# Kernel tuning notes

Hardware: AMD Instinct MI355X
Metric: run time of the kernel (lower is better)

The kernel has to match this reference:

```python
import jax, jax.numpy as jnp
import numpy as np

EPS = 1e-6
K = 20  # n_knn from init


def _vnt_weight(W):
    # VNT linear: rows normalized to sum to 1 (which_norm_VNT='norm') for translation equivariance
    return W / jnp.sum(W, axis=1, keepdims=True)


def _lin(W, x):
    # apply [out,in] weight over channel axis 1 of x: [B, C_in, 3, ...] -> [B, C_out, 3, ...]
    return jnp.einsum('oi,bi...->bo...', W, x)


def _vn_lrelu(x, Wf, Wd, vnt=False):
    # VN(T)LinearLeakyReLU with negative_slope=0.0, no batchnorm. Vector axis is axis 2.
    Wp = _vnt_weight(Wf) if vnt else Wf
    p = _lin(Wp, x)
    d = _lin(Wd, x)
    dot = jnp.sum(p * d, axis=2, keepdims=True)
    dsq = jnp.sum(d * d, axis=2, keepdims=True)
    return jnp.where(dot >= 0, p, p - (dot / (dsq + EPS)) * d)


def _knn(pts, k):
    # pts: [B,N,3] -> indices of k nearest (self included), via -||xi-xj||^2 top_k
    sq = jnp.sum(pts * pts, axis=-1)                      # [B,N]
    inner = jnp.einsum('bnd,bmd->bnm', pts, pts)          # [B,N,N]
    neg_dist = 2.0 * inner - sq[:, :, None] - sq[:, None, :]
    return jax.lax.top_k(neg_dist, k)[1]                  # [B,N,k]


def _graph_feature_cross(x, k):
    # x: [B,3,N] -> edge features [B, 3(feat: nbr-ctr, ctr, cross), 3(vec), N, k]
    pts = jnp.transpose(x, (0, 2, 1))                     # [B,N,3]
    idx = _knn(pts, k)                                    # [B,N,k]
    nbr = jax.vmap(lambda p, i: p[i])(pts, idx)           # [B,N,k,3]
    ctr = jnp.broadcast_to(pts[:, :, None, :], nbr.shape)
    cross = jnp.cross(nbr, ctr)
    feat = jnp.stack([nbr - ctr, ctr, cross], axis=3)     # [B,N,k,3feat,3vec]
    return jnp.transpose(feat, (0, 3, 4, 1, 2))           # [B,3feat,3vec,N,k]


def _forward(x, Wpos_f, Wpos_d, Wc1_f, Wc1_d, Wc2_f, Wc2_d, Wt_f, Wt_d, W1_f, W1_d, W2_f, W2_d, W3):
    feat = _graph_feature_cross(x, K)                     # [B,3,3,N,K]
    h = _vn_lrelu(feat, Wpos_f, Wpos_d, vnt=True)         # [B,64,3,N,K]
    h = h.mean(axis=-1)                                   # mean pool over k -> [B,64,3,N]
    x2 = _vn_lrelu(h, Wc1_f, Wc1_d, vnt=True)             # conv_center_
    xc = _vn_lrelu(x2, Wc2_f, Wc2_d, vnt=True)            # conv_center
    tx = _vn_lrelu(xc, Wt_f, Wt_d, vnt=True)              # conv_trans [B,12,3,N]
    trans_latent = tx.mean(axis=-1)                       # [B,12,3]
    h = h - xc                                            # center features
    h = _vn_lrelu(h, W1_f, W1_d)                          # conv1
    h = _vn_lrelu(h, W2_f, W2_d)                          # conv2
    h = _lin(W3, h)                                       # conv3 (plain VNLinear) [B,116,3,N]
    rot_latent = h.mean(axis=-1)                          # [B,116,3]
    return jnp.concatenate([rot_latent, trans_latent], axis=1)  # [B,128,3]


def setup_inputs() -> dict:
    key = jax.random.key(0)
    ks = jax.random.split(key, 16)
    B, N, C = 4, 4096, 64
    ROT = 116  # c_dim - trans_c_dim

    def w(k, o, i):
        return jax.random.normal(k, (o, i), jnp.float32) * 0.1

    def wt(k, o, i):
        # VNT weights: row sums kept near 1 so normalization is well-conditioned
        return jax.random.normal(k, (o, i), jnp.float32) * 0.02 + 1.0 / i

    return {
        'x': jax.random.normal(ks[0], (B, 3, N), jnp.float32),
        'Wpos_f': wt(ks[1], C, 3), 'Wpos_d': w(ks[2], C, 3),
        'Wc1_f': wt(ks[3], C, C), 'Wc1_d': w(ks[4], C, C),
        'Wc2_f': wt(ks[5], C, C), 'Wc2_d': w(ks[6], C, C),
        'Wt_f': wt(ks[7], 12, C), 'Wt_d': w(ks[8], 12, C),
        'W1_f': w(ks[9], C, C), 'W1_d': w(ks[10], C, C),
        'W2_f': w(ks[11], C, C), 'W2_d': w(ks[12], C, C),
        'W3': w(ks[13], ROT, C),
    }


def reference(x, Wpos_f, Wpos_d, Wc1_f, Wc1_d, Wc2_f, Wc2_d, Wt_f, Wt_d, W1_f, W1_d, W2_f, W2_d, W3):
    return _forward(x, Wpos_f, Wpos_d, Wc1_f, Wc1_d, Wc2_f, Wc2_d, Wt_f, Wt_d, W1_f, W1_d, W2_f, W2_d, W3)
```

## Files before the change

### kernel.cpp

```cpp
#include <hip/hip_runtime.h>

#define NPTS 4096
#define BATCH 4
#define KNN 20
#define ROT 116

__device__ __forceinline__ void vn_lrelu3(float p[3], const float d[3]) {
  float dot = p[0]*d[0] + p[1]*d[1] + p[2]*d[2];
  if (dot < 0.0f) {
    float dsq = d[0]*d[0] + d[1]*d[1] + d[2]*d[2];
    float r = dot / (dsq + 1e-6f);
    p[0] -= r*d[0]; p[1] -= r*d[1]; p[2] -= r*d[2];
  }
}

__global__ __launch_bounds__(256) void knn_kernel(const float* __restrict__ x,
                                                  int* __restrict__ knn) {
  const int row = blockIdx.x;
  const int b = row >> 12, i = row & (NPTS - 1);
  const float* __restrict__ xb = x + b * 3 * NPTS;
  const float cx = xb[i], cy = xb[NPTS + i], cz = xb[2 * NPTS + i];
  const int t = threadIdx.x;
  const int j0 = t << 4;

  __shared__ unsigned int hist[2048];
  __shared__ unsigned int ld_[384];
  __shared__ int lj_[384];
  __shared__ unsigned int lcount;
  __shared__ int s_B;
  __shared__ int wtot[4];

  for (int k = t; k < 2048; k += 256) hist[k] = 0u;
  if (t == 0) lcount = 0u;
  __syncthreads();

  unsigned int db[16];
#pragma unroll
  for (int q = 0; q < 4; ++q) {
    const float4 px = *(const float4*)(xb + j0 + 4 * q);
    const float4 py = *(const float4*)(xb + NPTS + j0 + 4 * q);
    const float4 pz = *(const float4*)(xb + 2 * NPTS + j0 + 4 * q);
    float dx, dy, dz, dd;
    dx = px.x - cx; dy = py.x - cy; dz = pz.x - cz;
    dd = dx*dx + dy*dy + dz*dz; db[4*q+0] = __float_as_uint(dd);
    dx = px.y - cx; dy = py.y - cy; dz = pz.y - cz;
    dd = dx*dx + dy*dy + dz*dz; db[4*q+1] = __float_as_uint(dd);
    dx = px.z - cx; dy = py.z - cy; dz = pz.z - cz;
    dd = dx*dx + dy*dy + dz*dz; db[4*q+2] = __float_as_uint(dd);
    dx = px.w - cx; dy = py.w - cy; dz = pz.w - cz;
    dd = dx*dx + dy*dy + dz*dz; db[4*q+3] = __float_as_uint(dd);
  }
#pragma unroll
  for (int s = 0; s < 16; ++s) atomicAdd(&hist[db[s] >> 20], 1u);
  __syncthreads();

  int v = 0;
#pragma unroll
  for (int s = 0; s < 8; ++s) v += (int)hist[t * 8 + s];
  const int myps = v;
  const int lane = t & 63;
#pragma unroll
  for (int off = 1; off < 64; off <<= 1) {
    int n = __shfl_up(v, off);
    if (lane >= off) v += n;
  }
  if (lane == 63) wtot[t >> 6] = v;
  __syncthreads();
  int woff = 0;
#pragma unroll
  for (int w = 0; w < 4; ++w) if (w < (t >> 6)) woff += wtot[w];
  const int cum_in = v + woff;
  const int cum_ex = cum_in - myps;
  if (cum_ex < KNN && cum_in >= KNN) {
    int cum = cum_ex, B = t * 8;
    for (int s = 0; s < 8; ++s) {
      const int hh = (int)hist[t * 8 + s];
      if (cum + hh >= KNN) { B = t * 8 + s; break; }
      cum += hh;
    }
    s_B = B;
  }
  __syncthreads();
  const unsigned int Bb = (unsigned int)s_B;
#pragma unroll
  for (int s = 0; s < 16; ++s) {
    if ((db[s] >> 20) <= Bb) {
      unsigned int pos = atomicAdd(&lcount, 1u);
      if (pos < 384u) { ld_[pos] = db[s]; lj_[pos] = j0 + s; }
    }
  }
  __syncthreads();
  const int n = min((int)lcount, 384);
  for (int idx = t; idx < n; idx += 256) {
    const unsigned int kd = ld_[idx]; const int kj = lj_[idx];
    int rank = 0;
    for (int m = 0; m < n; ++m) {
      const unsigned int md = ld_[m];
      rank += (md < kd || (md == kd && lj_[m] < kj)) ? 1 : 0;
    }
    if (rank < KNN) knn[row * KNN + rank] = kj;
  }
}

__global__ __launch_bounds__(256) void edge_kernel(const float* __restrict__ x,
                                                   const int* __restrict__ knn,
                                                   const float* __restrict__ Wf,
                                                   const float* __restrict__ Wd,
                                                   float* __restrict__ h) {
  const int g = threadIdx.x >> 6;
  const int lane = threadIdx.x & 63;
  const int p = (blockIdx.x << 2) + g;
  const int b = p >> 12, i = p & (NPTS - 1);
  const float* xb = x + b * 3 * NPTS;
  const float cx = xb[i], cy = xb[NPTS + i], cz = xb[2 * NPTS + i];
  __shared__ float e[4][KNN][3][3];
  if (lane < KNN) {
    int j = knn[p * KNN + lane];
    float nx = xb[j], ny = xb[NPTS + j], nz = xb[2 * NPTS + j];
    e[g][lane][0][0] = nx - cx; e[g][lane][0][1] = ny - cy; e[g][lane][0][2] = nz - cz;
    e[g][lane][1][0] = cx;      e[g][lane][1][1] = cy;      e[g][lane][1][2] = cz;
    e[g][lane][2][0] = ny * cz - nz * cy;
    e[g][lane][2][1] = nz * cx - nx * cz;
    e[g][lane][2][2] = nx * cy - ny * cx;
  }
  __syncthreads();
  const int c = lane;
  float f0 = Wf[c * 3 + 0], f1 = Wf[c * 3 + 1], f2 = Wf[c * 3 + 2];
  float s = 1.0f / (f0 + f1 + f2);
  f0 *= s; f1 *= s; f2 *= s;
  const float d0 = Wd[c * 3 + 0], d1 = Wd[c * 3 + 1], d2 = Wd[c * 3 + 2];
  float a0 = 0.f, a1 = 0.f, a2 = 0.f;
  for (int k = 0; k < KNN; ++k) {
    float pv[3], dv[3];
#pragma unroll
    for (int v = 0; v < 3; ++v) {
      pv[v] = f0 * e[g][k][0][v] + f1 * e[g][k][1][v] + f2 * e[g][k][2][v];
      dv[v] = d0 * e[g][k][0][v] + d1 * e[g][k][1][v] + d2 * e[g][k][2][v];
    }
    vn_lrelu3(pv, dv);
    a0 += pv[0]; a1 += pv[1]; a2 += pv[2];
  }
  const float inv = 1.0f / KNN;
  float* hp = h + p * 192 + c * 3;
  hp[0] = a0 * inv; hp[1] = a1 * inv; hp[2] = a2 * inv;
}

template<bool VNT, int MODE>
__global__ __launch_bounds__(256) void layer_batch(
    const float* in, float* out, float* aux,
    const float* __restrict__ Wf, const float* __restrict__ Wd) {
  __shared__ float wfT[64][65], wdT[64][65];
  __shared__ float act[4][4][64][4];
  const int t = threadIdx.x, q = t >> 6, c = t & 63;
  for (int e = t; e < 4096; e += 256) {
    wfT[e & 63][e >> 6] = Wf[e];
    wdT[e & 63][e >> 6] = Wd[e];
  }
  __syncthreads();
  if (VNT) {
    if (t < 64) {
      float s = 0.f;
      for (int i = 0; i < 64; ++i) s += wfT[i][t];
      s = 1.0f / s;
      for (int i = 0; i < 64; ++i) wfT[i][t] *= s;
    }
    __syncthreads();
  }
  const int pbase = (blockIdx.x * 4 + q) * 8;
  float r0 = 0.f, r1 = 0.f, r2 = 0.f;
  for (int pass = 0; pass < 2; ++pass) {
    const int p0 = pbase + pass * 4;
#pragma unroll
    for (int p = 0; p < 4; ++p) {
      const float* ip = in + (size_t)(p0 + p) * 192 + c * 3;
      *(float4*)act[q][p][c] = make_float4(ip[0], ip[1], ip[2], 0.f);
    }
    __builtin_amdgcn_wave_barrier();
    float af[12], ad[12];
#pragma unroll
    for (int e = 0; e < 12; ++e) { af[e] = 0.f; ad[e] = 0.f; }
    for (int i = 0; i < 64; ++i) {
      const float wfv = wfT[i][c];
      const float wdv = wdT[i][c];
#pragma unroll
      for (int p = 0; p < 4; ++p) {
        const float4 hv = *(const float4*)act[q][p][i];
        af[p*3+0] += wfv * hv.x; af[p*3+1] += wfv * hv.y; af[p*3+2] += wfv * hv.z;
        ad[p*3+0] += wdv * hv.x; ad[p*3+1] += wdv * hv.y; ad[p*3+2] += wdv * hv.z;
      }
    }
    __builtin_amdgcn_wave_barrier();
#pragma unroll
    for (int p = 0; p < 4; ++p) {
      float pf[3] = { af[p*3+0], af[p*3+1], af[p*3+2] };
      float pd[3] = { ad[p*3+0], ad[p*3+1], ad[p*3+2] };
      vn_lrelu3(pf, pd);
      const size_t ofs = (size_t)(p0 + p) * 192 + c * 3;
      if (MODE == 0) {
        out[ofs+0] = pf[0]; out[ofs+1] = pf[1]; out[ofs+2] = pf[2];
      } else if (MODE == 1) {
        const float h0 = aux[ofs+0], h1 = aux[ofs+1], h2 = aux[ofs+2];
        aux[ofs+0] = h0 - pf[0]; aux[ofs+1] = h1 - pf[1]; aux[ofs+2] = h2 - pf[2];
        out[ofs+0] = pf[0]; out[ofs+1] = pf[1]; out[ofs+2] = pf[2];
      } else {
        r0 += pf[0]; r1 += pf[1]; r2 += pf[2];
      }
    }
    __builtin_amdgcn_wave_barrier();
  }
  if (MODE == 2) {
    *(float4*)act[q][0][c] = make_float4(r0, r1, r2, 0.f);
    __syncthreads();
    if (t < 192) {
      const int cc = t / 3, vv = t - cc * 3;
      out[blockIdx.x * 192 + t] =
          act[0][0][cc][vv] + act[1][0][cc][vv] + act[2][0][cc][vv] + act[3][0][cc][vv];
    }
  }
}

__global__ __launch_bounds__(256) void trans_kernel(
    const float* __restrict__ xc,
    const float* __restrict__ Wtf, const float* __restrict__ Wtd,
    float* __restrict__ trans_part) {
  __shared__ float wtf[12][65], wtd[12][65];
  __shared__ float xpt[4][64][4];
  __shared__ float tred[4][12][3];
  const int t = threadIdx.x, q = t >> 6, l = t & 63;
  for (int e = t; e < 768; e += 256) {
    wtf[e >> 6][e & 63] = Wtf[e]; wtd[e >> 6][e & 63] = Wtd[e];
  }
  __syncthreads();
  if (t < 12) {
    float s = 0.f;
    for (int i = 0; i < 64; ++i) s += wtf[t][i];
    s = 1.0f / s;
    for (int i = 0; i < 64; ++i) wtf[t][i] *= s;
  }
  __syncthreads();
  const int cch = l >> 2, v = l & 3;
  const bool act = (cch < 12) && (v < 3);
  float ta = 0.f;
  const int pbase = (blockIdx.x * 4 + q) * 8;
  for (int g = 0; g < 8; ++g) {
    const float* xp = xc + (size_t)(pbase + g) * 192 + l * 3;
    xpt[q][l][0] = xp[0]; xpt[q][l][1] = xp[1]; xpt[q][l][2] = xp[2];
    __builtin_amdgcn_wave_barrier();
    float pf = 0.f, pd = 0.f;
    if (act) {
      for (int i = 0; i < 64; ++i) {
        const float a = xpt[q][i][v];
        pf += wtf[cch][i] * a;
        pd += wtd[cch][i] * a;
      }
    }
    float pp = pf * pd, dd = pd * pd;
    pp += __shfl_xor(pp, 1); pp += __shfl_xor(pp, 2);
    dd += __shfl_xor(dd, 1); dd += __shfl_xor(dd, 2);
    if (pp < 0.f) pf -= (pp / (dd + 1e-6f)) * pd;
    ta += pf;
    __builtin_amdgcn_wave_barrier();
  }
  if (act) { tred[q][cch][v] = ta; }
  __syncthreads();
  if (t < 36) {
    const int cc = t / 3, vv = t - cc * 3;
    trans_part[blockIdx.x * 36 + t] =
        tred[0][cc][vv] + tred[1][cc][vv] + tred[2][cc][vv] + tred[3][cc][vv];
  }
}

__global__ __launch_bounds__(384) void finalize_kernel(const float* __restrict__ rot_part,
                                                       const float* __restrict__ trans_part,
                                                       const float* __restrict__ W3,
                                                       float* __restrict__ out) {
  const int b = blockIdx.x;
  const int t = threadIdx.x;
  __shared__ float hsum[64][3];
  if (t < 192) {
    float s = 0.f;
    for (int blk = 0; blk < 128; ++blk)
      s += rot_part[(b * 128 + blk) * 192 + t];
    hsum[t / 3][t % 3] = s * (1.0f / NPTS);
  } else if (t < 228) {
    const int tt = t - 192;
    float s = 0.f;
    for (int blk = 0; blk < 128; ++blk)
      s += trans_part[(b * 128 + blk) * 36 + tt];
    out[b * 384 + 348 + tt] = s * (1.0f / NPTS);
  }
  __syncthreads();
  if (t < 348) {
    const int ch = t / 3, v = t - ch * 3;
    float s = 0.f;
    for (int i = 0; i < 64; ++i) s += W3[ch * 64 + i] * hsum[i][v];
    out[b * 384 + t] = s;
  }
}

extern "C" void kernel_launch(void* const* d_in, const int* in_sizes, int n_in,
                              void* d_out, int out_size, void* d_ws, size_t ws_size,
                              hipStream_t stream) {
  (void)in_sizes; (void)n_in; (void)out_size; (void)ws_size;
  const float* x     = (const float*)d_in[0];
  const float* Wposf = (const float*)d_in[1];
  const float* Wposd = (const float*)d_in[2];
  const float* Wc1f  = (const float*)d_in[3];
  const float* Wc1d  = (const float*)d_in[4];
  const float* Wc2f  = (const float*)d_in[5];
  const float* Wc2d  = (const float*)d_in[6];
  const float* Wtf   = (const float*)d_in[7];
  const float* Wtd   = (const float*)d_in[8];
  const float* W1f   = (const float*)d_in[9];
  const float* W1d   = (const float*)d_in[10];
  const float* W2f   = (const float*)d_in[11];
  const float* W2d   = (const float*)d_in[12];
  const float* W3    = (const float*)d_in[13];
  float* out = (float*)d_out;

  char* ws = (char*)d_ws;
  int*   knn        = (int*)ws;
  float* P          = (float*)(ws + 1310720);
  float* Q          = (float*)(ws + 13893632);
  float* trans_part = (float*)(ws + 26476544);
  float* rot_part   = (float*)(ws + 26550272);

  knn_kernel<<<BATCH * NPTS, 256, 0, stream>>>(x, knn);
  edge_kernel<<<BATCH * NPTS / 4, 256, 0, stream>>>(x, knn, Wposf, Wposd, P);
  layer_batch<true, 0><<<512, 256, 0, stream>>>(P, Q, nullptr, Wc1f, Wc1d);
  layer_batch<true, 1><<<512, 256, 0, stream>>>(Q, Q, P, Wc2f, Wc2d);
  trans_kernel<<<512, 256, 0, stream>>>(Q, Wtf, Wtd, trans_part);
  layer_batch<false, 0><<<512, 256, 0, stream>>>(P, P, nullptr, W1f, W1d);
  layer_batch<false, 2><<<512, 256, 0, stream>>>(P, rot_part, nullptr, W2f, W2d);
  finalize_kernel<<<BATCH, 384, 0, stream>>>(rot_part, trans_part, W3, out);
}
```

Measured before the change: 213.7 us.

## Fuse kNN selection and edge-feature layer into one kernel

Merges the kNN kernel and the edge-conv kernel so each block finds its point's 20 neighbours in shared memory and immediately computes the 64-channel VNT edge layer and k-mean. The neighbour indices no longer go through a global buffer, and one kernel launch is removed. Inside a block the 256 threads split the 20 neighbours into 4 groups of 5 and reduce partial sums through shared memory. Shared memory per block grows slightly, which may lower occupancy of the kNN-heavy kernel.

```diff
diff --git a/kernel.cpp b/kernel.cpp
--- a/kernel.cpp
+++ b/kernel.cpp
@@ -14,8 +14,10 @@
   }
 }
 
-__global__ __launch_bounds__(256) void knn_kernel(const float* __restrict__ x,
-                                                  int* __restrict__ knn) {
+__global__ __launch_bounds__(256) void knn_edge_kernel(const float* __restrict__ x,
+                                                       const float* __restrict__ Wf,
+                                                       const float* __restrict__ Wd,
+                                                       float* __restrict__ h) {
   const int row = blockIdx.x;
   const int b = row >> 12, i = row & (NPTS - 1);
   const float* __restrict__ xb = x + b * 3 * NPTS;
@@ -29,6 +31,9 @@
   __shared__ unsigned int lcount;
   __shared__ int s_B;
   __shared__ int wtot[4];
+  __shared__ int s_nbr[KNN];
+  __shared__ float e[KNN][3][3];
+  __shared__ float part[4][64][3];
 
   for (int k = t; k < 2048; k += 256) hist[k] = 0u;
   if (t == 0) lcount = 0u;
@@ -98,51 +103,48 @@
       const unsigned int md = ld_[m];
       rank += (md < kd || (md == kd && lj_[m] < kj)) ? 1 : 0;
     }
-    if (rank < KNN) knn[row * KNN + rank] = kj;
-  }
-}
-
-__global__ __launch_bounds__(256) void edge_kernel(const float* __restrict__ x,
-                                                   const int* __restrict__ knn,
-                                                   const float* __restrict__ Wf,
-                                                   const float* __restrict__ Wd,
-                                                   float* __restrict__ h) {
-  const int g = threadIdx.x >> 6;
-  const int lane = threadIdx.x & 63;
-  const int p = (blockIdx.x << 2) + g;
-  const int b = p >> 12, i = p & (NPTS - 1);
-  const float* xb = x + b * 3 * NPTS;
-  const float cx = xb[i], cy = xb[NPTS + i], cz = xb[2 * NPTS + i];
-  __shared__ float e[4][KNN][3][3];
-  if (lane < KNN) {
-    int j = knn[p * KNN + lane];
-    float nx = xb[j], ny = xb[NPTS + j], nz = xb[2 * NPTS + j];
-    e[g][lane][0][0] = nx - cx; e[g][lane][0][1] = ny - cy; e[g][lane][0][2] = nz - cz;
-    e[g][lane][1][0] = cx;      e[g][lane][1][1] = cy;      e[g][lane][1][2] = cz;
-    e[g][lane][2][0] = ny * cz - nz * cy;
-    e[g][lane][2][1] = nz * cx - nx * cz;
-    e[g][lane][2][2] = nx * cy - ny * cx;
-  }
-  __syncthreads();
-  const int c = lane;
+    if (rank < KNN) s_nbr[rank] = kj;
+  }
+  __syncthreads();
+
+  if (t < KNN) {
+    const int j = s_nbr[t];
+    const float nx = xb[j], ny = xb[NPTS + j], nz = xb[2 * NPTS + j];
+    e[t][0][0] = nx - cx; e[t][0][1] = ny - cy; e[t][0][2] = nz - cz;
+    e[t][1][0] = cx;      e[t][1][1] = cy;      e[t][1][2] = cz;
+    e[t][2][0] = ny * cz - nz * cy;
+    e[t][2][1] = nz * cx - nx * cz;
+    e[t][2][2] = nx * cy - ny * cx;
+  }
+  __syncthreads();
+
+  const int c = t & 63, kg = t >> 6;
   float f0 = Wf[c * 3 + 0], f1 = Wf[c * 3 + 1], f2 = Wf[c * 3 + 2];
-  float s = 1.0f / (f0 + f1 + f2);
+  const float s = 1.0f / (f0 + f1 + f2);
   f0 *= s; f1 *= s; f2 *= s;
   const float d0 = Wd[c * 3 + 0], d1 = Wd[c * 3 + 1], d2 = Wd[c * 3 + 2];
   float a0 = 0.f, a1 = 0.f, a2 = 0.f;
-  for (int k = 0; k < KNN; ++k) {
+#pragma unroll
+  for (int kk = 0; kk < 5; ++kk) {
+    const int k = kg * 5 + kk;
     float pv[3], dv[3];
 #pragma unroll
-    for (int v = 0; v < 3; ++v) {
-      pv[v] = f0 * e[g][k][0][v] + f1 * e[g][k][1][v] + f2 * e[g][k][2][v];
-      dv[v] = d0 * e[g][k][0][v] + d1 * e[g][k][1][v] + d2 * e[g][k][2][v];
+    for (int vv = 0; vv < 3; ++vv) {
+      pv[vv] = f0 * e[k][0][vv] + f1 * e[k][1][vv] + f2 * e[k][2][vv];
+      dv[vv] = d0 * e[k][0][vv] + d1 * e[k][1][vv] + d2 * e[k][2][vv];
     }
     vn_lrelu3(pv, dv);
     a0 += pv[0]; a1 += pv[1]; a2 += pv[2];
   }
-  const float inv = 1.0f / KNN;
-  float* hp = h + p * 192 + c * 3;
-  hp[0] = a0 * inv; hp[1] = a1 * inv; hp[2] = a2 * inv;
+  part[kg][c][0] = a0; part[kg][c][1] = a1; part[kg][c][2] = a2;
+  __syncthreads();
+  if (t < 64) {
+    const float inv = 1.0f / KNN;
+    float* hp = h + (size_t)row * 192 + t * 3;
+#pragma unroll
+    for (int vv = 0; vv < 3; ++vv)
+      hp[vv] = (part[0][t][vv] + part[1][t][vv] + part[2][t][vv] + part[3][t][vv]) * inv;
+  }
 }
 
 template<bool VNT, int MODE>
@@ -319,14 +321,12 @@
   float* out = (float*)d_out;
 
   char* ws = (char*)d_ws;
-  int*   knn        = (int*)ws;
   float* P          = (float*)(ws + 1310720);
   float* Q          = (float*)(ws + 13893632);
   float* trans_part = (float*)(ws + 26476544);
   float* rot_part   = (float*)(ws + 26550272);
 
-  knn_kernel<<<BATCH * NPTS, 256, 0, stream>>>(x, knn);
-  edge_kernel<<<BATCH * NPTS / 4, 256, 0, stream>>>(x, knn, Wposf, Wposd, P);
+  knn_edge_kernel<<<BATCH * NPTS, 256, 0, stream>>>(x, Wposf, Wposd, P);
   layer_batch<true, 0><<<512, 256, 0, stream>>>(P, Q, nullptr, Wc1f, Wc1d);
   layer_batch<true, 1><<<512, 256, 0, stream>>>(Q, Q, P, Wc2f, Wc2d);
   trans_kernel<<<512, 256, 0, stream>>>(Q, Wtf, Wtd, trans_part);
```

After: 214.3 us. About the same (+0.3%).
